# Performance work log

Hardware: AMD Instinct MI355X
Metric: run time of the kernel (lower is better)

Reference implementation:

```python
import jax, jax.numpy as jnp
import numpy as np

B, T, F_IN = 256, 168, 128
H = 512            # encoder hidden per direction; decoder hidden = 2H
OUT = 1
L_OUT = 48
SCALE = 0.05


def _lstm_scan(x, Wih, Whh, b, h0, c0):
    # x: [T, B, F]; PyTorch LSTM gate order i, f, g, o
    def step(carry, xt):
        h, c = carry
        g = xt @ Wih.T + h @ Whh.T + b
        i, f, gg, o = jnp.split(g, 4, axis=-1)
        c = jax.nn.sigmoid(f) * c + jax.nn.sigmoid(i) * jnp.tanh(gg)
        h = jax.nn.sigmoid(o) * jnp.tanh(c)
        return (h, c), h
    (hT, cT), ys = jax.lax.scan(step, (h0, c0), x)
    return ys, hT, cT


def setup_inputs() -> dict:
    key = jax.random.key(0)
    ks = jax.random.split(key, 16)
    r = lambda k, shp: (jax.random.normal(k, shp, dtype=jnp.float32) * SCALE)
    return {
        "input_seq": jax.random.normal(ks[0], (B, T, F_IN), dtype=jnp.float32),
        "enc_Wih_f": r(ks[1], (4 * H, F_IN)),
        "enc_Whh_f": r(ks[2], (4 * H, H)),
        "enc_bih_f": r(ks[3], (4 * H,)),
        "enc_bhh_f": r(ks[4], (4 * H,)),
        "enc_Wih_b": r(ks[5], (4 * H, F_IN)),
        "enc_Whh_b": r(ks[6], (4 * H, H)),
        "enc_bih_b": r(ks[7], (4 * H,)),
        "enc_bhh_b": r(ks[8], (4 * H,)),
        "dec_Wih": r(ks[9], (4 * 2 * H, OUT)),
        "dec_Whh": r(ks[10], (4 * 2 * H, 2 * H)),
        "dec_bih": r(ks[11], (4 * 2 * H,)),
        "dec_bhh": r(ks[12], (4 * 2 * H,)),
        "fc_W": r(ks[13], (OUT, 2 * H)),
        "fc_b": r(ks[14], (OUT,)),
        "output_length": L_OUT,
    }


def reference(input_seq, enc_Wih_f, enc_Whh_f, enc_bih_f, enc_bhh_f,
              enc_Wih_b, enc_Whh_b, enc_bih_b, enc_bhh_b,
              dec_Wih, dec_Whh, dec_bih, dec_bhh, fc_W, fc_b, output_length):
    b = input_seq.shape[0]
    h = enc_Whh_f.shape[1]
    x = jnp.transpose(input_seq, (1, 0, 2))  # [T, B, F]
    h0 = jnp.zeros((b, h), input_seq.dtype)
    c0 = jnp.zeros((b, h), input_seq.dtype)
    # bidirectional encoder (final hidden/cell only are used downstream)
    _, hf, cf = _lstm_scan(x, enc_Wih_f, enc_Whh_f, enc_bih_f + enc_bhh_f, h0, c0)
    _, hb, cb = _lstm_scan(x[::-1], enc_Wih_b, enc_Whh_b, enc_bih_b + enc_bhh_b, h0, c0)
    # _cat_hidden: concat fwd/bwd states along feature dim -> decoder init state [B, 2H]
    hd = jnp.concatenate([hf, hb], axis=-1)
    cd = jnp.concatenate([cf, cb], axis=-1)
    bd = dec_bih + dec_bhh
    x0 = jnp.zeros((b, fc_W.shape[0]), input_seq.dtype)  # initial decoder input = zeros

    def dec_step(carry, _):
        hh, cc, xt = carry
        g = xt @ dec_Wih.T + hh @ dec_Whh.T + bd
        i, f, gg, o = jnp.split(g, 4, axis=-1)
        cc = jax.nn.sigmoid(f) * cc + jax.nn.sigmoid(i) * jnp.tanh(gg)
        hh = jax.nn.sigmoid(o) * jnp.tanh(cc)
        pred = hh @ fc_W.T + fc_b  # [B, OUT]
        return (hh, cc, pred), pred

    _, preds = jax.lax.scan(dec_step, (hd, cd, x0), None, length=output_length)
    # [L, B, OUT] -> [B, L, OUT] -> squeeze(dim=2) with OUT==1 -> [B, L]
    return jnp.transpose(preds, (1, 0, 2)).squeeze(2)
```

## Files before the change

kernel.cpp:

```cpp
#include <hip/hip_runtime.h>


constexpr int B_ = 256, T_ = 168, F_ = 128, H_ = 512, L_ = 48;
constexpr int KE = F_ + H_;
constexpr int HD = 1024;
constexpr int GE = 4 * H_;
constexpr int EPAD = KE + 8;
constexpr int DPAD = HD + 8;

constexpr int FL256_IDX = 0;
constexpr int CLAIM_IDX = 256;
constexpr int ENCF_IDX  = 768;
constexpr int DECF_IDX  = 1280;

constexpr size_t OFF_SYNC = 0;
constexpr size_t OFF_WCF = 8192;
constexpr size_t OFF_WCB = OFF_WCF + (size_t)GE * KE * 2;
constexpr size_t OFF_PP  = OFF_WCB + (size_t)GE * KE * 2;
constexpr size_t OFF_BF  = OFF_PP  + (size_t)8 * 2 * 64 * 32 * 4;
constexpr size_t OFF_BB  = OFF_BF  + (size_t)GE * 4;
constexpr size_t OFF_XH  = OFF_BB  + (size_t)GE * 4;
constexpr size_t OFF_HE  = OFF_XH  + (size_t)T_ * B_ * F_ * 2;
constexpr size_t OFF_HDD = OFF_HE  + (size_t)2 * 2 * B_ * H_ * 2;
constexpr size_t OFF_CD  = OFF_HDD + (size_t)2 * B_ * HD * 2;

using h8 = __attribute__((ext_vector_type(8))) _Float16;
using f4 = __attribute__((ext_vector_type(4))) float;
using u4 = __attribute__((ext_vector_type(4))) unsigned;

#define DEV static __device__ __forceinline__

DEV float sigm(float x)  { return __fdividef(1.f, 1.f + __expf(-x)); }
DEV float tanh_(float x) { return 1.f - __fdividef(2.f, __expf(2.f * x) + 1.f); }

DEV h8 as_h8(f4 v) { union { f4 f; h8 h; } u; u.f = v; return u.h; }

DEV void astore_u64(void* p, unsigned long long v) {
  __hip_atomic_store((unsigned long long*)p, v, __ATOMIC_RELAXED,
                     __HIP_MEMORY_SCOPE_AGENT);
}
DEV void astore_u32(void* p, unsigned v) {
  __hip_atomic_store((unsigned*)p, v, __ATOMIC_RELAXED, __HIP_MEMORY_SCOPE_AGENT);
}
DEV unsigned aload_u32(const void* p) {
  return __hip_atomic_load((const unsigned*)p, __ATOMIC_RELAXED,
                           __HIP_MEMORY_SCOPE_AGENT);
}
DEV float aload_f32(const void* p) {
  return __hip_atomic_load((const float*)p, __ATOMIC_RELAXED,
                           __HIP_MEMORY_SCOPE_AGENT);
}
DEV void astore_f32(void* p, float v) {
  __hip_atomic_store((float*)p, v, __ATOMIC_RELAXED, __HIP_MEMORY_SCOPE_AGENT);
}
DEV void astore_u16(void* p, _Float16 v) {
  union { _Float16 h; unsigned short s; } u; u.h = v;
  __hip_atomic_store((unsigned short*)p, u.s, __ATOMIC_RELAXED,
                     __HIP_MEMORY_SCOPE_AGENT);
}
DEV void vm_drain() { asm volatile("s_waitcnt vmcnt(0)" ::: "memory"); }

template<bool DEEP>
DEV void ld16(const _Float16* p, f4* A) {
#define L16(FL) asm volatile( \
    "global_load_dwordx4 %0,  %16, off" FL "\n\t" \
    "global_load_dwordx4 %1,  %16, off offset:64" FL "\n\t" \
    "global_load_dwordx4 %2,  %16, off offset:128" FL "\n\t" \
    "global_load_dwordx4 %3,  %16, off offset:192" FL "\n\t" \
    "global_load_dwordx4 %4,  %16, off offset:256" FL "\n\t" \
    "global_load_dwordx4 %5,  %16, off offset:320" FL "\n\t" \
    "global_load_dwordx4 %6,  %16, off offset:384" FL "\n\t" \
    "global_load_dwordx4 %7,  %16, off offset:448" FL "\n\t" \
    "global_load_dwordx4 %8,  %16, off offset:512" FL "\n\t" \
    "global_load_dwordx4 %9,  %16, off offset:576" FL "\n\t" \
    "global_load_dwordx4 %10, %16, off offset:640" FL "\n\t" \
    "global_load_dwordx4 %11, %16, off offset:704" FL "\n\t" \
    "global_load_dwordx4 %12, %16, off offset:768" FL "\n\t" \
    "global_load_dwordx4 %13, %16, off offset:832" FL "\n\t" \
    "global_load_dwordx4 %14, %16, off offset:896" FL "\n\t" \
    "global_load_dwordx4 %15, %16, off offset:960" FL "\n\t" \
    "s_waitcnt vmcnt(0)" \
    : "=&v"(A[0]),"=&v"(A[1]),"=&v"(A[2]),"=&v"(A[3]),"=&v"(A[4]),"=&v"(A[5]), \
      "=&v"(A[6]),"=&v"(A[7]),"=&v"(A[8]),"=&v"(A[9]),"=&v"(A[10]),"=&v"(A[11]), \
      "=&v"(A[12]),"=&v"(A[13]),"=&v"(A[14]),"=&v"(A[15]) \
    : "v"(p) : "memory")
  if constexpr (DEEP) { L16(" sc0 sc1"); } else { L16(" sc0"); }
#undef L16
}

template<bool DEEP>
DEV void ld32(const _Float16* p, f4* A) {
#define L32(FL) asm volatile( \
    "global_load_dwordx4 %0,  %32, off" FL "\n\t" \
    "global_load_dwordx4 %1,  %32, off offset:64" FL "\n\t" \
    "global_load_dwordx4 %2,  %32, off offset:128" FL "\n\t" \
    "global_load_dwordx4 %3,  %32, off offset:192" FL "\n\t" \
    "global_load_dwordx4 %4,  %32, off offset:256" FL "\n\t" \
    "global_load_dwordx4 %5,  %32, off offset:320" FL "\n\t" \
    "global_load_dwordx4 %6,  %32, off offset:384" FL "\n\t" \
    "global_load_dwordx4 %7,  %32, off offset:448" FL "\n\t" \
    "global_load_dwordx4 %8,  %32, off offset:512" FL "\n\t" \
    "global_load_dwordx4 %9,  %32, off offset:576" FL "\n\t" \
    "global_load_dwordx4 %10, %32, off offset:640" FL "\n\t" \
    "global_load_dwordx4 %11, %32, off offset:704" FL "\n\t" \
    "global_load_dwordx4 %12, %32, off offset:768" FL "\n\t" \
    "global_load_dwordx4 %13, %32, off offset:832" FL "\n\t" \
    "global_load_dwordx4 %14, %32, off offset:896" FL "\n\t" \
    "global_load_dwordx4 %15, %32, off offset:960" FL "\n\t" \
    "global_load_dwordx4 %16, %32, off offset:1024" FL "\n\t" \
    "global_load_dwordx4 %17, %32, off offset:1088" FL "\n\t" \
    "global_load_dwordx4 %18, %32, off offset:1152" FL "\n\t" \
    "global_load_dwordx4 %19, %32, off offset:1216" FL "\n\t" \
    "global_load_dwordx4 %20, %32, off offset:1280" FL "\n\t" \
    "global_load_dwordx4 %21, %32, off offset:1344" FL "\n\t" \
    "global_load_dwordx4 %22, %32, off offset:1408" FL "\n\t" \
    "global_load_dwordx4 %23, %32, off offset:1472" FL "\n\t" \
    "global_load_dwordx4 %24, %32, off offset:1536" FL "\n\t" \
    "global_load_dwordx4 %25, %32, off offset:1600" FL "\n\t" \
    "global_load_dwordx4 %26, %32, off offset:1664" FL "\n\t" \
    "global_load_dwordx4 %27, %32, off offset:1728" FL "\n\t" \
    "global_load_dwordx4 %28, %32, off offset:1792" FL "\n\t" \
    "global_load_dwordx4 %29, %32, off offset:1856" FL "\n\t" \
    "global_load_dwordx4 %30, %32, off offset:1920" FL "\n\t" \
    "global_load_dwordx4 %31, %32, off offset:1984" FL "\n\t" \
    "s_waitcnt vmcnt(0)" \
    : "=&v"(A[0]),"=&v"(A[1]),"=&v"(A[2]),"=&v"(A[3]),"=&v"(A[4]),"=&v"(A[5]), \
      "=&v"(A[6]),"=&v"(A[7]),"=&v"(A[8]),"=&v"(A[9]),"=&v"(A[10]),"=&v"(A[11]), \
      "=&v"(A[12]),"=&v"(A[13]),"=&v"(A[14]),"=&v"(A[15]),"=&v"(A[16]),"=&v"(A[17]), \
      "=&v"(A[18]),"=&v"(A[19]),"=&v"(A[20]),"=&v"(A[21]),"=&v"(A[22]),"=&v"(A[23]), \
      "=&v"(A[24]),"=&v"(A[25]),"=&v"(A[26]),"=&v"(A[27]),"=&v"(A[28]),"=&v"(A[29]), \
      "=&v"(A[30]),"=&v"(A[31]) \
    : "v"(p) : "memory")
  if constexpr (DEEP) { L32(" sc0 sc1"); } else { L32(" sc0"); }
#undef L32
}

template<bool DEEP>
DEV void ld16s(const float* p, float* v) {
#define L16S(FL) asm volatile( \
    "global_load_dword %0,  %16, off" FL "\n\t" \
    "global_load_dword %1,  %16, off offset:128" FL "\n\t" \
    "global_load_dword %2,  %16, off offset:256" FL "\n\t" \
    "global_load_dword %3,  %16, off offset:384" FL "\n\t" \
    "global_load_dword %4,  %16, off offset:512" FL "\n\t" \
    "global_load_dword %5,  %16, off offset:640" FL "\n\t" \
    "global_load_dword %6,  %16, off offset:768" FL "\n\t" \
    "global_load_dword %7,  %16, off offset:896" FL "\n\t" \
    "global_load_dword %8,  %16, off offset:1024" FL "\n\t" \
    "global_load_dword %9,  %16, off offset:1152" FL "\n\t" \
    "global_load_dword %10, %16, off offset:1280" FL "\n\t" \
    "global_load_dword %11, %16, off offset:1408" FL "\n\t" \
    "global_load_dword %12, %16, off offset:1536" FL "\n\t" \
    "global_load_dword %13, %16, off offset:1664" FL "\n\t" \
    "global_load_dword %14, %16, off offset:1792" FL "\n\t" \
    "global_load_dword %15, %16, off offset:1920" FL "\n\t" \
    "s_waitcnt vmcnt(0)" \
    : "=&v"(v[0]),"=&v"(v[1]),"=&v"(v[2]),"=&v"(v[3]),"=&v"(v[4]),"=&v"(v[5]), \
      "=&v"(v[6]),"=&v"(v[7]),"=&v"(v[8]),"=&v"(v[9]),"=&v"(v[10]),"=&v"(v[11]), \
      "=&v"(v[12]),"=&v"(v[13]),"=&v"(v[14]),"=&v"(v[15]) \
    : "v"(p) : "memory")
  if constexpr (DEEP) { L16S(" sc0 sc1"); } else { L16S(" sc0"); }
#undef L16S
}

DEV unsigned pollflag(const unsigned* p, bool deep) {
  unsigned v;
  if (deep)
    asm volatile("global_load_dword %0, %1, off sc0 sc1\n\t"
                 "s_waitcnt vmcnt(0)" : "=&v"(v) : "v"(p) : "memory");
  else
    asm volatile("global_load_dword %0, %1, off sc0\n\t"
                 "s_waitcnt vmcnt(0)" : "=&v"(v) : "v"(p) : "memory");
  return v;
}

DEV void wait_ge_block(const unsigned* p, unsigned target, bool deep, int cap,
                       int wave) {
  if (wave == 0) {
    for (int it = 0; it < cap; ++it) {
      unsigned v = pollflag(p, deep);
      if (__ballot(v >= target) == ~0ull) break;
    }
  }
  __syncthreads();
}

DEV void gsync(unsigned* fl, int bi, unsigned phase, int tid) {
  vm_drain();
  __syncthreads();
  if (tid == 0) astore_u32(fl + bi, phase);
  if (tid < 64) {
    const unsigned* p = fl + tid * 4;
    for (int it = 0; it < (1 << 20); ++it) {
      u4 v;
      asm volatile("global_load_dwordx4 %0, %1, off sc0 sc1\n\t"
                   "s_waitcnt vmcnt(0)" : "=&v"(v) : "v"(p) : "memory");
      unsigned a = v[0] < v[1] ? v[0] : v[1];
      unsigned b = v[2] < v[3] ? v[2] : v[3];
      if (__ballot((a < b ? a : b) >= phase) == ~0ull) break;
    }
  }
  __syncthreads();
  asm volatile("" ::: "memory");
}

__global__ void prep_misc(const float* bihF, const float* bhhF,
                          const float* bihB, const float* bhhB, char* ws) {
  int i = blockIdx.x * blockDim.x + threadIdx.x;
  if (i < 1024) astore_u64(ws + (size_t)i * 8, 0ull);
  if (i < GE) {
    ((float*)(ws + OFF_BF))[i] = bihF[i] + bhhF[i];
    ((float*)(ws + OFF_BB))[i] = bihB[i] + bhhB[i];
  }
  if (i < 2 * 2 * B_ * H_ / 4) astore_u64((char*)ws + OFF_HE + (size_t)i * 8, 0ull);
}

__global__ void conv_encw(const float* WihF, const float* WhhF,
                          const float* WihB, const float* WhhB, char* ws) {
  int i = blockIdx.x * blockDim.x + threadIdx.x;
  if (i >= GE * KE) return;
  int r = i / KE, k = i - r * KE;
  float vF = (k < F_) ? WihF[r * F_ + k] : WhhF[r * H_ + (k - F_)];
  float vB = (k < F_) ? WihB[r * F_ + k] : WhhB[r * H_ + (k - F_)];
  ((_Float16*)(ws + OFF_WCF))[i] = (_Float16)vF;
  ((_Float16*)(ws + OFF_WCB))[i] = (_Float16)vB;
}

__global__ void conv_x(const float* x, char* ws) {
  int i = blockIdx.x * blockDim.x + threadIdx.x;
  if (i >= T_ * B_ * F_) return;
  int f = i & 127, b = (i >> 7) & 255, t = i >> 15;
  ((_Float16*)(ws + OFF_XH))[i] = (_Float16)x[((size_t)b * T_ + t) * F_ + f];
}

template<bool LOCAL>
DEV void encoder_phase(int dir, int chunk, int slice,
                       int tid, int wave, int quad, int col, int lane,
                       char* ws, _Float16* lds, _Float16 (*htile)[16]) {
  const _Float16* Wenc  = (const _Float16*)(ws + (dir ? OFF_WCB : OFF_WCF));
  const float*    biasE = (const float*)(ws + (dir ? OFF_BB : OFF_BF));
  const _Float16* Xh    = (const _Float16*)(ws + OFF_XH);
  _Float16* hE = (_Float16*)(ws + OFF_HE);
  _Float16* hD = (_Float16*)(ws + OFF_HDD);
  float*    cD = (float*)(ws + OFF_CD);
  unsigned* encf = (unsigned*)ws + ENCF_IDX + (dir * 4 + chunk) * 64;

  const int j0 = slice * 16;
  const int mb = chunk * 64;

  for (int it = 0; it < 20; ++it) {
    int idx = it * 256 + tid;
    int n = idx / 80, e = idx - n * 80;
    int g = n >> 4, u = n & 15;
    *((h8*)(lds + n * EPAD) + e) =
        *((const h8*)(Wenc + (size_t)(g * H_ + j0 + u) * KE) + e);
  }
  float breg[4];
#pragma unroll
  for (int g = 0; g < 4; ++g) breg[g] = biasE[g * H_ + j0 + col];
  float cst[4] = {0.f, 0.f, 0.f, 0.f};
  __syncthreads();

  h8 Bf[4][16];
#pragma unroll
  for (int g = 0; g < 4; ++g)
#pragma unroll
    for (int kk = 0; kk < 16; ++kk)
      Bf[g][kk] = *((const h8*)(lds + (g * 16 + col) * EPAD + F_) + kk * 4 + quad);

  const int arow = mb + wave * 16 + col;
  const int mrow = mb + wave * 16 + quad * 4;

  for (int t = 0; t < T_; ++t) {
    const int par = t & 1;
    const int tx  = dir ? (T_ - 1 - t) : t;
    f4 z = {0.f, 0.f, 0.f, 0.f};
    f4 acc[4] = {z, z, z, z};

    const h8* xr = (const h8*)(Xh + ((size_t)tx * B_ + arow) * F_);
#pragma unroll
    for (int kk = 0; kk < 4; ++kk) {
      h8 a = xr[kk * 4 + quad];
#pragma unroll
      for (int g = 0; g < 4; ++g) {
        h8 b = *((const h8*)(lds + (g * 16 + col) * EPAD) + kk * 4 + quad);
        acc[g] = __builtin_amdgcn_mfma_f32_16x16x32_f16(a, b, acc[g], 0, 0, 0);
      }
    }
    if (t > 0)
      wait_ge_block(encf + (lane & 31), (unsigned)t, !LOCAL, 1 << 16, wave);
    f4 A[16];
    ld16<!LOCAL>(hE + ((size_t)(par * 2 + dir) * B_ + arow) * H_ + quad * 8, A);
#pragma unroll
    for (int kk = 0; kk < 16; ++kk) {
      h8 a = as_h8(A[kk]);
#pragma unroll
      for (int g = 0; g < 4; ++g)
        acc[g] = __builtin_amdgcn_mfma_f32_16x16x32_f16(a, Bf[g][kk], acc[g], 0, 0, 0);
    }

#pragma unroll
    for (int r = 0; r < 4; ++r) {
      float gi = acc[0][r] + breg[0];
      float gf = acc[1][r] + breg[1];
      float gg = acc[2][r] + breg[2];
      float go = acc[3][r] + breg[3];
      float c = sigm(gf) * cst[r] + sigm(gi) * tanh_(gg);
      cst[r] = c;
      float h = sigm(go) * tanh_(c);
      htile[wave * 16 + quad * 4 + r][col] = (_Float16)h;
      if (t == T_ - 1)
        astore_f32(&cD[(size_t)(mrow + r) * HD + dir * H_ + j0 + col], c);
    }
    __syncthreads();
    if (tid < 128) {
      int row = tid >> 1, half = tid & 1;
      const unsigned long long* src =
          (const unsigned long long*)&htile[row][half * 8];
      if (t < T_ - 1) {
        _Float16* dst = hE + ((size_t)((par ^ 1) * 2 + dir) * B_ + mb + row) * H_ +
                        j0 + half * 8;
        if (LOCAL) {
          ((unsigned long long*)dst)[0] = src[0];
          ((unsigned long long*)(dst + 4))[0] = src[1];
        } else {
          astore_u64(dst, src[0]);
          astore_u64(dst + 4, src[1]);
        }
      } else {
        _Float16* dst = hD + (size_t)(mb + row) * HD + dir * H_ + j0 + half * 8;
        astore_u64(dst, src[0]);
        astore_u64(dst + 4, src[1]);
      }
    }
    vm_drain();
    __syncthreads();
    if (tid == 0 && t < T_ - 1) {
      if (LOCAL) *(volatile unsigned*)(encf + slice) = (unsigned)(t + 1);
      else       astore_u32(encf + slice, (unsigned)(t + 1));
    }
  }
}

DEV void decoder_phase(int xcd, int rank, int tid, int wave, int quad, int col,
                       int lane, const float* dWih, const float* dWhh,
                       const float* dbih, const float* dbhh, const float* fcW,
                       const float* fcb, float* out, char* ws, _Float16* lds,
                       float* predbuf) {
  _Float16* hdd = (_Float16*)(ws + OFF_HDD);
  float* cD = (float*)(ws + OFF_CD);
  float* PP = (float*)(ws + OFF_PP) + (size_t)xcd * 2 * 64 * 32;
  unsigned* decf = (unsigned*)ws + DECF_IDX + xcd * 64;

  const int j0b = rank * 32;
  const int R0  = xcd * 32;
  const int m   = wave & 1;
  const int uh  = wave >> 1;
  const int unit = j0b + uh * 16 + col;
  const int arow = R0 + m * 16 + col;
  const int mrow = R0 + m * 16 + quad * 4;

  for (int it = 0; it < 64; ++it) {
    int idx = it * 256 + tid;
    int n = idx >> 8, c = idx & 255;
    int srow = (n >> 5) * HD + j0b + (n & 31);
    f4 w = *((const f4*)(dWhh + (size_t)srow * HD + c * 4));
    union { _Float16 h[4]; unsigned long long q; } u2;
#pragma unroll
    for (int i2 = 0; i2 < 4; ++i2) u2.h[i2] = (_Float16)w[i2];
    *(unsigned long long*)(lds + n * DPAD + c * 4) = u2.q;
  }
  h8 Bf[2][32];
#pragma unroll
  for (int gg = 0; gg < 2; ++gg)
#pragma unroll
    for (int kk = 0; kk < 32; ++kk) {
      const float* src = dWhh + (size_t)((2 + gg) * HD + unit) * HD + kk * 32 + quad * 8;
      f4 w0 = *((const f4*)src);
      f4 w1 = *((const f4*)(src + 4));
      union { _Float16 h[8]; h8 v; } u3;
#pragma unroll
      for (int i2 = 0; i2 < 4; ++i2) {
        u3.h[i2]     = (_Float16)w0[i2];
        u3.h[4 + i2] = (_Float16)w1[i2];
      }
      Bf[gg][kk] = u3.v;
    }
  float breg[4], wreg[4];
#pragma unroll
  for (int g = 0; g < 4; ++g) {
    breg[g] = dbih[g * HD + unit] + dbhh[g * HD + unit];
    wreg[g] = dWih[g * HD + unit];
  }
  const float fcw = fcW[unit];
  const float fb  = fcb[0];
  float cst[4];
#pragma unroll
  for (int r = 0; r < 4; ++r)
    cst[r] = aload_f32(cD + (size_t)(mrow + r) * HD + unit);
  __syncthreads();

  for (int l = 0; l <= L_; ++l) {
    float predv = 0.f;
    if (l > 0) {
      wait_ge_block(decf + (lane & 31), (unsigned)l, true, 1 << 16, wave);
      const float* PPr = PP + (size_t)((l - 1) & 1) * 64 * 32;
      int row = lane & 31, halfsel = lane >> 5;
      const float* pb = PPr + (size_t)(halfsel * 32) * 32 + row;
      float pv[16], s = 0.f;
      ld16s<true>(pb, pv);
#pragma unroll
      for (int j = 0; j < 16; ++j) s += pv[j];
      ld16s<true>(pb + 16 * 32, pv);
#pragma unroll
      for (int j = 0; j < 16; ++j) s += pv[j];
      s += __shfl_xor(s, 32);
      predv = s + fb;
      if (rank == 0 && wave == 0 && lane < 32)
        predbuf[(l - 1) * 32 + lane] = predv;
    }
    if (l == L_) break;
    const int par = l & 1;

    f4 A[32];
    ld32<true>(hdd + ((size_t)par * B_ + arow) * HD + quad * 8, A);

    f4 z = {0.f, 0.f, 0.f, 0.f};
    f4 acc[4] = {z, z, z, z};
#pragma unroll
    for (int kk = 0; kk < 32; ++kk) {
      h8 a = as_h8(A[kk]);
      h8 b0 = *((const h8*)(lds + (0 * 32 + uh * 16 + col) * DPAD) + kk * 4 + quad);
      h8 b1 = *((const h8*)(lds + (1 * 32 + uh * 16 + col) * DPAD) + kk * 4 + quad);
      acc[0] = __builtin_amdgcn_mfma_f32_16x16x32_f16(a, b0, acc[0], 0, 0, 0);
      acc[1] = __builtin_amdgcn_mfma_f32_16x16x32_f16(a, b1, acc[1], 0, 0, 0);
      acc[2] = __builtin_amdgcn_mfma_f32_16x16x32_f16(a, Bf[0][kk], acc[2], 0, 0, 0);
      acc[3] = __builtin_amdgcn_mfma_f32_16x16x32_f16(a, Bf[1][kk], acc[3], 0, 0, 0);
    }

    float pr[4], sum[4];
#pragma unroll
    for (int r = 0; r < 4; ++r)
      pr[r] = (l > 0) ? __shfl(predv, m * 16 + quad * 4 + r) : 0.f;
#pragma unroll
    for (int r = 0; r < 4; ++r) {
      float gi = acc[0][r] + breg[0] + pr[r] * wreg[0];
      float gf = acc[1][r] + breg[1] + pr[r] * wreg[1];
      float gg = acc[2][r] + breg[2] + pr[r] * wreg[2];
      float go = acc[3][r] + breg[3] + pr[r] * wreg[3];
      float c = sigm(gf) * cst[r] + sigm(gi) * tanh_(gg);
      cst[r] = c;
      float h = sigm(go) * tanh_(c);
      size_t hoff = ((size_t)(par ^ 1) * B_ + mrow + r) * HD + unit;
      astore_u16(hdd + hoff, (_Float16)h);
      sum[r] = h * fcw;
    }
#pragma unroll
    for (int off = 1; off < 16; off <<= 1) {
#pragma unroll
      for (int r = 0; r < 4; ++r) sum[r] += __shfl_xor(sum[r], off, 16);
    }
    if (col == 0) {
      float* PPw = PP + (size_t)(l & 1) * 64 * 32;
      float* pdst = PPw + (size_t)(rank * 2 + uh) * 32 + m * 16 + quad * 4;
      union { float f[4]; unsigned long long q[2]; } u5;
#pragma unroll
      for (int r = 0; r < 4; ++r) u5.f[r] = sum[r];
      astore_u64(pdst, u5.q[0]);
      astore_u64(pdst + 2, u5.q[1]);
    }
    vm_drain();
    __syncthreads();
    if (tid == 0) astore_u32(decf + rank, (unsigned)(l + 1));
  }

  if (rank == 0) {
    __syncthreads();
    for (int idx = tid; idx < L_ * 32; idx += 256) {
      int row2 = idx & 31, st = idx >> 5;
      out[(size_t)(R0 + row2) * L_ + st] = predbuf[st * 32 + row2];
    }
  }
}

__global__ __launch_bounds__(256, 1)
void rnn_kernel(const float* __restrict__ dWih, const float* __restrict__ dWhh,
                const float* __restrict__ dbih, const float* __restrict__ dbhh,
                const float* __restrict__ fcW, const float* __restrict__ fcb,
                float* __restrict__ out, char* __restrict__ ws) {
  __shared__ __align__(16) _Float16 lds[64 * DPAD];
  __shared__ __align__(16) _Float16 htile[64][16];
  __shared__ __align__(16) float predbuf[L_ * 32];
  __shared__ int sh[2];

  const int tid  = threadIdx.x;
  const int wave = tid >> 6;
  const int lane = tid & 63;
  const int quad = lane >> 4;
  const int col  = lane & 15;
  const int bi   = blockIdx.x;

  unsigned* sync  = (unsigned*)(ws + OFF_SYNC);
  unsigned* fl    = sync + FL256_IDX;
  unsigned* claim = sync + CLAIM_IDX;

  if (tid == 0) {
    unsigned x;
    asm volatile("s_getreg_b32 %0, hwreg(HW_REG_XCC_ID)" : "=s"(x));
    int xcd = (int)(x & 7u);
    unsigned r = __hip_atomic_fetch_add(claim + xcd * 64, 1u, __ATOMIC_RELAXED,
                                        __HIP_MEMORY_SCOPE_AGENT);
    sh[0] = xcd;
    sh[1] = (int)r;
  }
  __syncthreads();
  const int xcd = sh[0], rank = sh[1];
  gsync(fl, bi, 1u, tid);
  if (tid == 0) {
    int d = 0;
    for (int k = 0; k < 8; ++k)
      if (aload_u32(claim + k * 64) != 32u) d = 1;
    sh[0] = d;
  }
  __syncthreads();
  const bool deg = (sh[0] != 0) || (rank >= 32);

  if (!deg)
    encoder_phase<true>(xcd >> 2, xcd & 3, rank, tid, wave, quad, col, lane,
                        ws, lds, htile);
  else
    encoder_phase<false>(bi >> 7, bi & 3, (bi & 127) >> 2, tid, wave, quad, col,
                         lane, ws, lds, htile);

  gsync(fl, bi, 2u, tid);

  if (!deg)
    decoder_phase(xcd, rank, tid, wave, quad, col, lane, dWih, dWhh,
                  dbih, dbhh, fcW, fcb, out, ws, lds, predbuf);
  else
    decoder_phase(bi >> 5, bi & 31, tid, wave, quad, col, lane, dWih,
                  dWhh, dbih, dbhh, fcW, fcb, out, ws, lds, predbuf);
}

extern "C" void kernel_launch(void* const* d_in, const int* in_sizes, int n_in,
                              void* d_out, int out_size, void* d_ws, size_t ws_size,
                              hipStream_t stream) {
  const float* x     = (const float*)d_in[0];
  const float* eWihF = (const float*)d_in[1];
  const float* eWhhF = (const float*)d_in[2];
  const float* ebihF = (const float*)d_in[3];
  const float* ebhhF = (const float*)d_in[4];
  const float* eWihB = (const float*)d_in[5];
  const float* eWhhB = (const float*)d_in[6];
  const float* ebihB = (const float*)d_in[7];
  const float* ebhhB = (const float*)d_in[8];
  const float* dWih  = (const float*)d_in[9];
  const float* dWhh  = (const float*)d_in[10];
  const float* dbih  = (const float*)d_in[11];
  const float* dbhh  = (const float*)d_in[12];
  const float* fcW   = (const float*)d_in[13];
  const float* fcb   = (const float*)d_in[14];
  float* out = (float*)d_out;
  char*  ws  = (char*)d_ws;

  prep_misc<<<512, 256, 0, stream>>>(ebihF, ebhhF, ebihB, ebhhB, ws);
  conv_encw<<<(GE * KE) / 256, 256, 0, stream>>>(eWihF, eWhhF, eWihB, eWhhB, ws);
  conv_x<<<(T_ * B_ * F_) / 256, 256, 0, stream>>>(x, ws);

  void* args[] = {(void*)&dWih, (void*)&dWhh, (void*)&dbih, (void*)&dbhh,
                  (void*)&fcW,  (void*)&fcb,  (void*)&out,  (void*)&ws};
  hipError_t err = hipLaunchCooperativeKernel(rnn_kernel, dim3(256), dim3(256),
                                              args, 0, stream);
  if (err != hipSuccess) {
    rnn_kernel<<<dim3(256), dim3(256), 0, stream>>>(dWih, dWhh, dbih, dbhh,
                                                    fcW, fcb, out, ws);
  }
}
```

Baseline: 1.512 ms.

## Split persistent RNN kernel into separate encoder and decoder launches with per-wave polling

Splits the single cooperative persistent kernel into an encoder kernel and a decoder kernel launched back to back. The decoder re-does XCD rank claiming and its own grid barrier using new sync slots. Per-step flag waits now poll in every wave instead of one wave followed by a block barrier. The split gives each kernel a smaller LDS footprint and drops the cooperative launch and the mid-kernel grid sync. In exchange it adds a kernel boundary, a second claim/barrier setup, and more polling traffic from all waves, and it relies on all 256 blocks being co-resident without a cooperative launch.

```diff
diff --git a/kernel.cpp b/kernel.cpp
--- a/kernel.cpp
+++ b/kernel.cpp
@@ -8,13 +8,15 @@
 constexpr int EPAD = KE + 8;
 constexpr int DPAD = HD + 8;
 
-constexpr int FL256_IDX = 0;
-constexpr int CLAIM_IDX = 256;
-constexpr int ENCF_IDX  = 768;
-constexpr int DECF_IDX  = 1280;
+constexpr int FL256_IDX  = 0;
+constexpr int CLAIM_IDX  = 256;
+constexpr int ENCF_IDX   = 768;
+constexpr int DECF_IDX   = 1280;
+constexpr int CLAIM2_IDX = 2048;
+constexpr int FL2_IDX    = 2560;
 
 constexpr size_t OFF_SYNC = 0;
-constexpr size_t OFF_WCF = 8192;
+constexpr size_t OFF_WCF = 16384;
 constexpr size_t OFF_WCB = OFF_WCF + (size_t)GE * KE * 2;
 constexpr size_t OFF_PP  = OFF_WCB + (size_t)GE * KE * 2;
 constexpr size_t OFF_BF  = OFF_PP  + (size_t)8 * 2 * 64 * 32 * 4;
@@ -173,16 +175,11 @@
                  "s_waitcnt vmcnt(0)" : "=&v"(v) : "v"(p) : "memory");
   return v;
 }
-
-DEV void wait_ge_block(const unsigned* p, unsigned target, bool deep, int cap,
-                       int wave) {
-  if (wave == 0) {
-    for (int it = 0; it < cap; ++it) {
-      unsigned v = pollflag(p, deep);
-      if (__ballot(v >= target) == ~0ull) break;
-    }
-  }
-  __syncthreads();
+DEV void wait_ge(const unsigned* p, unsigned target, bool deep, int cap) {
+  for (int it = 0; it < cap; ++it) {
+    unsigned v = pollflag(p, deep);
+    if (__ballot(v >= target) == ~0ull) return;
+  }
 }
 
 DEV void gsync(unsigned* fl, int bi, unsigned phase, int tid) {
@@ -207,7 +204,7 @@
 __global__ void prep_misc(const float* bihF, const float* bhhF,
                           const float* bihB, const float* bhhB, char* ws) {
   int i = blockIdx.x * blockDim.x + threadIdx.x;
-  if (i < 1024) astore_u64(ws + (size_t)i * 8, 0ull);
+  if (i < 2048) astore_u64(ws + (size_t)i * 8, 0ull);
   if (i < GE) {
     ((float*)(ws + OFF_BF))[i] = bihF[i] + bhhF[i];
     ((float*)(ws + OFF_BB))[i] = bihB[i] + bhhB[i];
@@ -288,7 +285,7 @@
       }
     }
     if (t > 0)
-      wait_ge_block(encf + (lane & 31), (unsigned)t, !LOCAL, 1 << 16, wave);
+      wait_ge(encf + (lane & 31), (unsigned)t, !LOCAL, 1 << 16);
     f4 A[16];
     ld16<!LOCAL>(hE + ((size_t)(par * 2 + dir) * B_ + arow) * H_ + quad * 8, A);
 #pragma unroll
@@ -403,7 +400,7 @@
   for (int l = 0; l <= L_; ++l) {
     float predv = 0.f;
     if (l > 0) {
-      wait_ge_block(decf + (lane & 31), (unsigned)l, true, 1 << 16, wave);
+      wait_ge(decf + (lane & 31), (unsigned)l, true, 1 << 16);
       const float* PPr = PP + (size_t)((l - 1) & 1) * 64 * 32;
       int row = lane & 31, halfsel = lane >> 5;
       const float* pb = PPr + (size_t)(halfsel * 32) * 32 + row;
@@ -484,13 +481,9 @@
 }
 
 __global__ __launch_bounds__(256, 1)
-void rnn_kernel(const float* __restrict__ dWih, const float* __restrict__ dWhh,
-                const float* __restrict__ dbih, const float* __restrict__ dbhh,
-                const float* __restrict__ fcW, const float* __restrict__ fcb,
-                float* __restrict__ out, char* __restrict__ ws) {
-  __shared__ __align__(16) _Float16 lds[64 * DPAD];
+void enc_kernel(char* __restrict__ ws) {
+  __shared__ __align__(16) _Float16 lds[64 * EPAD];
   __shared__ __align__(16) _Float16 htile[64][16];
-  __shared__ __align__(16) float predbuf[L_ * 32];
   __shared__ int sh[2];
 
   const int tid  = threadIdx.x;
@@ -531,8 +524,48 @@
   else
     encoder_phase<false>(bi >> 7, bi & 3, (bi & 127) >> 2, tid, wave, quad, col,
                          lane, ws, lds, htile);
-
-  gsync(fl, bi, 2u, tid);
+}
+
+__global__ __launch_bounds__(256, 1)
+void dec_kernel(const float* __restrict__ dWih, const float* __restrict__ dWhh,
+                const float* __restrict__ dbih, const float* __restrict__ dbhh,
+                const float* __restrict__ fcW, const float* __restrict__ fcb,
+                float* __restrict__ out, char* __restrict__ ws) {
+  __shared__ __align__(16) _Float16 lds[64 * DPAD];
+  __shared__ __align__(16) float predbuf[L_ * 32];
+  __shared__ int sh[2];
+
+  const int tid  = threadIdx.x;
+  const int wave = tid >> 6;
+  const int lane = tid & 63;
+  const int quad = lane >> 4;
+  const int col  = lane & 15;
+  const int bi   = blockIdx.x;
+
+  unsigned* sync  = (unsigned*)(ws + OFF_SYNC);
+  unsigned* fl2   = sync + FL2_IDX;
+  unsigned* claim = sync + CLAIM2_IDX;
+
+  if (tid == 0) {
+    unsigned x;
+    asm volatile("s_getreg_b32 %0, hwreg(HW_REG_XCC_ID)" : "=s"(x));
+    int xcd = (int)(x & 7u);
+    unsigned r = __hip_atomic_fetch_add(claim + xcd * 64, 1u, __ATOMIC_RELAXED,
+                                        __HIP_MEMORY_SCOPE_AGENT);
+    sh[0] = xcd;
+    sh[1] = (int)r;
+  }
+  __syncthreads();
+  const int xcd = sh[0], rank = sh[1];
+  gsync(fl2, bi, 1u, tid);
+  if (tid == 0) {
+    int d = 0;
+    for (int k = 0; k < 8; ++k)
+      if (aload_u32(claim + k * 64) != 32u) d = 1;
+    sh[0] = d;
+  }
+  __syncthreads();
+  const bool deg = (sh[0] != 0) || (rank >= 32);
 
   if (!deg)
     decoder_phase(xcd, rank, tid, wave, quad, col, lane, dWih, dWhh,
@@ -567,12 +600,7 @@
   conv_encw<<<(GE * KE) / 256, 256, 0, stream>>>(eWihF, eWhhF, eWihB, eWhhB, ws);
   conv_x<<<(T_ * B_ * F_) / 256, 256, 0, stream>>>(x, ws);
 
-  void* args[] = {(void*)&dWih, (void*)&dWhh, (void*)&dbih, (void*)&dbhh,
-                  (void*)&fcW,  (void*)&fcb,  (void*)&out,  (void*)&ws};
-  hipError_t err = hipLaunchCooperativeKernel(rnn_kernel, dim3(256), dim3(256),
-                                              args, 0, stream);
-  if (err != hipSuccess) {
-    rnn_kernel<<<dim3(256), dim3(256), 0, stream>>>(dWih, dWhh, dbih, dbhh,
-                                                    fcW, fcb, out, ws);
-  }
-}
+  enc_kernel<<<dim3(256), dim3(256), 0, stream>>>(ws);
+  dec_kernel<<<dim3(256), dim3(256), 0, stream>>>(dWih, dWhh, dbih, dbhh,
+                                                  fcW, fcb, out, ws);
+}
```

Result: faster. 1.440 ms (-4.8%).
